# Performance work log

Measured on AMD Instinct MI355X. Metric: run time of the kernel, lower is better.

Reference implementation:

```python
import jax, jax.numpy as jnp
import numpy as np

B, T, M = 4, 1024, 512
H, K, V = 8, 64, 64
EPS = 1e-6


def setup_inputs() -> dict:
    key = jax.random.key(0)
    ks = jax.random.split(key, 8)
    s = 1.0 / np.sqrt(M)
    return {
        "query": jax.random.normal(ks[0], (B, T, M), jnp.float32),
        "key": jax.random.normal(ks[1], (B, T, M), jnp.float32),
        "value": jax.random.normal(ks[2], (B, T, M), jnp.float32),
        "Wq": jax.random.normal(ks[3], (M, H * K), jnp.float32) * s,
        "Wk": jax.random.normal(ks[4], (M, H * K), jnp.float32) * s,
        "Wv": jax.random.normal(ks[5], (M, H * V), jnp.float32) * s,
        # gate linear is zero-initialized in the original (Constant(0.0)); use
        # small random weights so the gate path is exercised numerically.
        "Wg": jax.random.normal(ks[6], (M, H * V), jnp.float32) * (0.02 * s),
        "bg": jnp.zeros((H * V,), jnp.float32),
        "Wo": jax.random.normal(ks[7], (H * V, M), jnp.float32) * (1.0 / np.sqrt(H * V)),
    }


def _phi(x):
    return jax.nn.elu(x) + 1.0


def reference(query, key, value, Wq, Wk, Wv, Wg, bg, Wo):
    # projections -> [B, T, H, d]
    q = (query @ Wq).reshape(B, T, H, K)
    k = (key @ Wk).reshape(B, T, H, K)
    v = (value @ Wv).reshape(B, T, H, V)

    qf = _phi(q)
    kf = _phi(k)

    # multiplicative value gate from the raw value input
    gate = jax.nn.sigmoid((value @ Wg + bg).reshape(B, T, H, V))
    v = v * (2.0 * gate)

    # visualization attention map: qf . kf, causal, row-normalized
    scores = jnp.einsum("bthk,bshk->bhts", qf, kf)  # [B,H,T,T]
    causal = (jnp.arange(T)[None, :] <= jnp.arange(T)[:, None]).astype(scores.dtype)
    scores = scores * causal[None, None]
    att_map = scores / (jnp.sum(scores, axis=-1, keepdims=True) + EPS)

    # causal linear attention via cumulative sums (Tq == Tk so the idx-take
    # in the original is an identity gather)
    kv = jnp.einsum("bthk,bthv->bthkv", kf, v)  # [B,T,H,K,V]
    kv_cum = jnp.cumsum(kv, axis=1)
    k_cum = jnp.cumsum(kf, axis=1)               # [B,T,H,K]

    numer = jnp.einsum("bthk,bthkv->bthv", qf, kv_cum)
    denom = jnp.einsum("bthk,bthk->bth", qf, k_cum) + EPS
    out = (numer / denom[..., None]).reshape(B, T, H * V)
    out = out @ Wo  # [B,T,M]
    return out, att_map
```

## Files before the change

### kernel.cpp

```cpp
#include <hip/hip_runtime.h>
#include <cstdint>

#define TDIM 1024
#define BDIM 4
#define EPSF 1e-6f

#define OFF_INV   0u
#define OFF_KSUM  32768u
#define OFF_KV    65536u
#define FLOAT_BYTES 8650752u
#define UOFF_QP 0u
#define UOFF_KP 2097152u
#define UOFF_VP 4194304u
#define UOFF_NB 6291456u
#define UOFF_WQ 8388608u
#define UOFF_WK 8650752u
#define UOFF_WV 8912896u
#define UOFF_WG 9175040u
#define UOFF_WO 9437184u

typedef short bf16x8 __attribute__((ext_vector_type(8)));
typedef float f32x4  __attribute__((ext_vector_type(4)));
typedef unsigned short ushort_t;

union bfu { int4 i4; unsigned short us[8]; bf16x8 v; };

__device__ __forceinline__ float phi_f(float x)  { return x > 0.f ? x + 1.f : __expf(x); }
__device__ __forceinline__ float sigm_f(float x) { return 1.f / (1.f + __expf(-x)); }
__device__ __forceinline__ unsigned short f2b(float x) {
    union { float f; unsigned u; } v; v.f = x;
    return (unsigned short)((v.u + 0x7FFFu + ((v.u >> 16) & 1u)) >> 16);
}
__device__ __forceinline__ float b2f(unsigned short s) {
    union { unsigned u; float f; } v; v.u = (unsigned)s << 16; return v.f;
}
__device__ __forceinline__ int4 pack8(float4 a, float4 b) {
    bfu u;
    u.us[0] = f2b(a.x); u.us[1] = f2b(a.y); u.us[2] = f2b(a.z); u.us[3] = f2b(a.w);
    u.us[4] = f2b(b.x); u.us[5] = f2b(b.y); u.us[6] = f2b(b.z); u.us[7] = f2b(b.w);
    return u.i4;
}
#define FMA4(ACC, S, V) do { (ACC).x += (S)*(V).x; (ACC).y += (S)*(V).y; \
                             (ACC).z += (S)*(V).z; (ACC).w += (S)*(V).w; } while (0)

__global__ __launch_bounds__(256) void castwt_all(const float* __restrict__ W0,
                                                  const float* __restrict__ W1,
                                                  const float* __restrict__ W2,
                                                  const float* __restrict__ W3,
                                                  const float* __restrict__ W4,
                                                  ushort_t* __restrict__ T0,
                                                  ushort_t* __restrict__ T1,
                                                  ushort_t* __restrict__ T2,
                                                  ushort_t* __restrict__ T3,
                                                  ushort_t* __restrict__ T4) {
    const float* W; ushort_t* Wt;
    switch (blockIdx.z) {
        case 0: W = W0; Wt = T0; break;
        case 1: W = W1; Wt = T1; break;
        case 2: W = W2; Wt = T2; break;
        case 3: W = W3; Wt = T3; break;
        default: W = W4; Wt = T4; break;
    }
    __shared__ unsigned short tile[32][36];
    const int t = threadIdx.x;
    const int r0 = blockIdx.y * 32, c0 = blockIdx.x * 32;
    {
        const int r = t >> 3, c4 = (t & 7) * 4;
        float4 x = *(const float4*)(W + (size_t)(r0 + r) * 512 + c0 + c4);
        tile[c4 + 0][r] = f2b(x.x); tile[c4 + 1][r] = f2b(x.y);
        tile[c4 + 2][r] = f2b(x.z); tile[c4 + 3][r] = f2b(x.w);
    }
    __syncthreads();
    const int c = t >> 3, r4 = (t & 7) * 4;
    ushort4 o;
    o.x = tile[c][r4 + 0]; o.y = tile[c][r4 + 1];
    o.z = tile[c][r4 + 2]; o.w = tile[c][r4 + 3];
    *(ushort4*)(Wt + (size_t)(c0 + c) * 512 + r0 + r4) = o;
}

__global__ __launch_bounds__(256) void proj_k(const float* __restrict__ query,
                                              const float* __restrict__ key_,
                                              const float* __restrict__ value,
                                              const ushort_t* __restrict__ wqt,
                                              const ushort_t* __restrict__ wkt,
                                              const ushort_t* __restrict__ wvt,
                                              const ushort_t* __restrict__ wgt,
                                              const float* __restrict__ bg,
                                              ushort_t* __restrict__ qp,
                                              ushort_t* __restrict__ kp,
                                              ushort_t* __restrict__ vp) {
    __shared__ __align__(16) unsigned short As[2][4096];
    __shared__ __align__(16) unsigned short Bs[2][4096];
    __shared__ __align__(16) unsigned short Bs2[2][4096];
    const int z = blockIdx.z;
    const float* A = (z == 0) ? query : (z == 1) ? key_ : value;
    const ushort_t* B0 = (z == 0) ? wqt : (z == 1) ? wkt : wvt;
    ushort_t* outp = (z == 0) ? qp : (z == 1) ? kp : vp;
    const bool dual = (z == 2);

    const int tid = threadIdx.x;
    const int row0 = blockIdx.x * 64, n0 = blockIdx.y * 64;
    const int w = tid >> 6, lane = tid & 63;
    const int cc = tid & 7, rr = tid >> 3;
    const int fm = lane & 15, fq = lane >> 4;
    const int la0 = (cc * 64 + (rr ^ cc)) * 8;
    const int la1 = (cc * 64 + ((rr + 32) ^ cc)) * 8;

    f32x4 acc[4], acc2[4];
#pragma unroll
    for (int i = 0; i < 4; i++) {
        acc[i]  = (f32x4){0.f, 0.f, 0.f, 0.f};
        acc2[i] = (f32x4){0.f, 0.f, 0.f, 0.f};
    }

    const float*   aptr = A  + (size_t)(row0 + rr) * 512 + cc * 8;
    const ushort_t* bptr = B0 + (size_t)(n0 + rr) * 512 + cc * 8;
    const ushort_t* gptr = wgt + (size_t)(n0 + rr) * 512 + cc * 8;

    float4 a0 = *(const float4*)(aptr);
    float4 a1 = *(const float4*)(aptr + 4);
    float4 a2 = *(const float4*)(aptr + 32 * 512);
    float4 a3 = *(const float4*)(aptr + 32 * 512 + 4);
    int4 b0 = *(const int4*)(bptr);
    int4 b1 = *(const int4*)(bptr + 32 * 512);
    int4 g0 = {0, 0, 0, 0}, g1 = {0, 0, 0, 0};
    if (dual) { g0 = *(const int4*)(gptr); g1 = *(const int4*)(gptr + 32 * 512); }
    *(int4*)&As[0][la0] = pack8(a0, a1);
    *(int4*)&As[0][la1] = pack8(a2, a3);
    *(int4*)&Bs[0][la0] = b0; *(int4*)&Bs[0][la1] = b1;
    if (dual) { *(int4*)&Bs2[0][la0] = g0; *(int4*)&Bs2[0][la1] = g1; }
    __syncthreads();

    for (int kti = 0; kti < 8; kti++) {
        const int buf = kti & 1;
        if (kti < 7) {
            const int off = (kti + 1) * 64;
            a0 = *(const float4*)(aptr + off);
            a1 = *(const float4*)(aptr + off + 4);
            a2 = *(const float4*)(aptr + off + 32 * 512);
            a3 = *(const float4*)(aptr + off + 32 * 512 + 4);
            b0 = *(const int4*)(bptr + off);
            b1 = *(const int4*)(bptr + off + 32 * 512);
            if (dual) {
                g0 = *(const int4*)(gptr + off);
                g1 = *(const int4*)(gptr + off + 32 * 512);
            }
        }
        if (dual) {
#pragma unroll
            for (int j = 0; j < 2; j++) {
                const int cu = j * 4 + fq;
                bf16x8 af = *(const bf16x8*)&As[buf][(cu * 64 + ((w * 16 + fm) ^ cu)) * 8];
#pragma unroll
                for (int nb = 0; nb < 4; nb++) {
                    bf16x8 bv = *(const bf16x8*)&Bs[buf][(cu * 64 + ((nb * 16 + fm) ^ cu)) * 8];
                    bf16x8 gv = *(const bf16x8*)&Bs2[buf][(cu * 64 + ((nb * 16 + fm) ^ cu)) * 8];
                    acc[nb]  = __builtin_amdgcn_mfma_f32_16x16x32_bf16(af, bv, acc[nb], 0, 0, 0);
                    acc2[nb] = __builtin_amdgcn_mfma_f32_16x16x32_bf16(af, gv, acc2[nb], 0, 0, 0);
                }
            }
        } else {
#pragma unroll
            for (int j = 0; j < 2; j++) {
                const int cu = j * 4 + fq;
                bf16x8 af = *(const bf16x8*)&As[buf][(cu * 64 + ((w * 16 + fm) ^ cu)) * 8];
#pragma unroll
                for (int nb = 0; nb < 4; nb++) {
                    bf16x8 bv = *(const bf16x8*)&Bs[buf][(cu * 64 + ((nb * 16 + fm) ^ cu)) * 8];
                    acc[nb] = __builtin_amdgcn_mfma_f32_16x16x32_bf16(af, bv, acc[nb], 0, 0, 0);
                }
            }
        }
        if (kti < 7) {
            const int nb_ = buf ^ 1;
            *(int4*)&As[nb_][la0] = pack8(a0, a1);
            *(int4*)&As[nb_][la1] = pack8(a2, a3);
            *(int4*)&Bs[nb_][la0] = b0; *(int4*)&Bs[nb_][la1] = b1;
            if (dual) { *(int4*)&Bs2[nb_][la0] = g0; *(int4*)&Bs2[nb_][la1] = g1; }
            __syncthreads();
        }
    }

#pragma unroll
    for (int nb = 0; nb < 4; nb++) {
        const int col = n0 + nb * 16 + fm;
        const float bb = dual ? bg[col] : 0.f;
#pragma unroll
        for (int r = 0; r < 4; r++) {
            const int row = row0 + w * 16 + fq * 4 + r;
            const float v = acc[nb][r];
            const ushort_t o = dual ? f2b(v * 2.f * sigm_f(acc2[nb][r] + bb))
                                    : f2b(phi_f(v));
            outp[(size_t)row * 512 + col] = o;
        }
    }
}

__global__ __launch_bounds__(256) void outproj_k(const ushort_t* __restrict__ A,
                                                 const ushort_t* __restrict__ Bt,
                                                 float* __restrict__ out) {
    __shared__ __align__(16) unsigned short As[2][4096];
    __shared__ __align__(16) unsigned short Bs[2][4096];
    const int tid = threadIdx.x;
    const int row0 = blockIdx.x * 64, n0 = blockIdx.y * 64;
    const int w = tid >> 6, lane = tid & 63;
    const int cc = tid & 7, rr = tid >> 3;
    const int fm = lane & 15, fq = lane >> 4;
    const int la0 = (cc * 64 + (rr ^ cc)) * 8;
    const int la1 = (cc * 64 + ((rr + 32) ^ cc)) * 8;

    f32x4 acc[4];
#pragma unroll
    for (int i = 0; i < 4; i++) acc[i] = (f32x4){0.f, 0.f, 0.f, 0.f};

    const ushort_t* aptr = A  + (size_t)(row0 + rr) * 512 + cc * 8;
    const ushort_t* bptr = Bt + (size_t)(n0 + rr) * 512 + cc * 8;
    int4 ra0 = *(const int4*)(aptr);
    int4 ra1 = *(const int4*)(aptr + 32 * 512);
    int4 rb0 = *(const int4*)(bptr);
    int4 rb1 = *(const int4*)(bptr + 32 * 512);
    *(int4*)&As[0][la0] = ra0; *(int4*)&As[0][la1] = ra1;
    *(int4*)&Bs[0][la0] = rb0; *(int4*)&Bs[0][la1] = rb1;
    __syncthreads();

    for (int kti = 0; kti < 8; kti++) {
        const int buf = kti & 1;
        if (kti < 7) {
            const int off = (kti + 1) * 64;
            ra0 = *(const int4*)(aptr + off);
            ra1 = *(const int4*)(aptr + off + 32 * 512);
            rb0 = *(const int4*)(bptr + off);
            rb1 = *(const int4*)(bptr + off + 32 * 512);
        }
#pragma unroll
        for (int j = 0; j < 2; j++) {
            const int cu = j * 4 + fq;
            bf16x8 af = *(const bf16x8*)&As[buf][(cu * 64 + ((w * 16 + fm) ^ cu)) * 8];
#pragma unroll
            for (int nb = 0; nb < 4; nb++) {
                bf16x8 bv = *(const bf16x8*)&Bs[buf][(cu * 64 + ((nb * 16 + fm) ^ cu)) * 8];
                acc[nb] = __builtin_amdgcn_mfma_f32_16x16x32_bf16(af, bv, acc[nb], 0, 0, 0);
            }
        }
        if (kti < 7) {
            const int nb_ = buf ^ 1;
            *(int4*)&As[nb_][la0] = ra0; *(int4*)&As[nb_][la1] = ra1;
            *(int4*)&Bs[nb_][la0] = rb0; *(int4*)&Bs[nb_][la1] = rb1;
            __syncthreads();
        }
    }
#pragma unroll
    for (int nb = 0; nb < 4; nb++) {
        const int col = n0 + nb * 16 + fm;
#pragma unroll
        for (int r = 0; r < 4; r++) {
            const int row = row0 + w * 16 + fq * 4 + r;
            __builtin_nontemporal_store(acc[nb][r], &out[(size_t)row * 512 + col]);
        }
    }
}

__global__ __launch_bounds__(256) void chunksum_k(const ushort_t* __restrict__ kb,
                                                  const ushort_t* __restrict__ vb,
                                                  float* __restrict__ kv,
                                                  float* __restrict__ ksum) {
    __shared__ __align__(16) float kf_c[64][68];
    __shared__ __align__(16) float vg_c[64][68];
    const int tid = threadIdx.x;
    const int bh = blockIdx.x, c = blockIdx.y;
    const int b = bh >> 3, h = bh & 7;
    const int r = tid >> 2, qq = tid & 3;
    {
        const size_t rowbase = ((size_t)(b * TDIM + c * 64 + r)) * 512 + h * 64 + qq * 16;
        bfu k0, k1, v0, v1;
        k0.i4 = *(const int4*)(kb + rowbase);
        k1.i4 = *(const int4*)(kb + rowbase + 8);
        v0.i4 = *(const int4*)(vb + rowbase);
        v1.i4 = *(const int4*)(vb + rowbase + 8);
#pragma unroll
        for (int j = 0; j < 8; j++) {
            kf_c[r][qq * 16 + j]     = b2f(k0.us[j]);
            kf_c[r][qq * 16 + 8 + j] = b2f(k1.us[j]);
            vg_c[r][qq * 16 + j]     = b2f(v0.us[j]);
            vg_c[r][qq * 16 + 8 + j] = b2f(v1.us[j]);
        }
    }
    __syncthreads();
    const int k0i = (tid >> 4) * 4;
    const int v0i = (tid & 15) * 4;
    float4 a4[4];
#pragma unroll
    for (int i = 0; i < 4; i++) a4[i] = make_float4(0.f, 0.f, 0.f, 0.f);
    for (int t = 0; t < 64; t++) {
        float4 kk4 = *(const float4*)&kf_c[t][k0i];
        float4 vv  = *(const float4*)&vg_c[t][v0i];
        FMA4(a4[0], kk4.x, vv); FMA4(a4[1], kk4.y, vv);
        FMA4(a4[2], kk4.z, vv); FMA4(a4[3], kk4.w, vv);
    }
    const size_t base = (size_t)(bh * 16 + c) * 64;
#pragma unroll
    for (int i = 0; i < 4; i++)
        *(float4*)(kv + (base + k0i + i) * 64 + v0i) = a4[i];
    if (tid < 64) {
        float s = 0.f;
        for (int t = 0; t < 64; t++) s += kf_c[t][tid];
        ksum[base + tid] = s;
    }
}

__global__ __launch_bounds__(256) void fused_k(const ushort_t* __restrict__ qb,
                                               const ushort_t* __restrict__ kb,
                                               const ushort_t* __restrict__ vb,
                                               const float* __restrict__ kvc,
                                               const float* __restrict__ ksum,
                                               ushort_t* __restrict__ nbo,
                                               float* __restrict__ invw) {
    __shared__ __align__(16) unsigned short qs[4096];
    __shared__ __align__(16) unsigned short ksb[4096];
    __shared__ __align__(16) unsigned short vrow[64 * 72];
    __shared__ __align__(16) float kvf[64 * 68];
    __shared__ __align__(16) float sc[64 * 68];
    __shared__ float kpre[64];
    __shared__ float ps[256];
    __shared__ float inv_s[64];

    const int tid = threadIdx.x;
    const int bh = blockIdx.x, diag = 15 - (int)blockIdx.y;
    const int tt0 = diag * 64;
    const int b = bh >> 3, h = bh & 7;
    const int w = tid >> 6, lane = tid & 63;
    const int fm = lane & 15, fq = lane >> 4;
    const int rr = tid >> 3, cc = tid & 7;
    const int la0 = (cc * 64 + (rr ^ cc)) * 8;
    const int la1 = (cc * 64 + ((rr + 32) ^ cc)) * 8;

    {
        const ushort_t* qptr = qb + ((size_t)(b * TDIM + tt0 + rr)) * 512 + h * 64 + cc * 8;
        *(int4*)&qs[la0] = *(const int4*)qptr;
        *(int4*)&qs[la1] = *(const int4*)(qptr + 32 * 512);
        const ushort_t* kptr = kb + ((size_t)(b * TDIM + tt0 + rr)) * 512 + h * 64 + cc * 8;
        *(int4*)&ksb[la0] = *(const int4*)kptr;
        *(int4*)&ksb[la1] = *(const int4*)(kptr + 32 * 512);
        const int r = tid >> 2, qq = tid & 3;
        const ushort_t* vptr = vb + ((size_t)(b * TDIM + tt0 + r)) * 512 + h * 64 + qq * 16;
        *(int4*)&vrow[r * 72 + qq * 16]     = *(const int4*)vptr;
        *(int4*)&vrow[r * 72 + qq * 16 + 8] = *(const int4*)(vptr + 8);
        float4 a4[4];
#pragma unroll
        for (int u = 0; u < 4; u++) a4[u] = make_float4(0.f, 0.f, 0.f, 0.f);
        for (int c2 = 0; c2 < diag; c2++) {
            const float* p = kvc + (size_t)(bh * 16 + c2) * 4096 + r * 64 + qq * 16;
#pragma unroll
            for (int u = 0; u < 4; u++) {
                float4 x = *(const float4*)(p + 4 * u);
                a4[u].x += x.x; a4[u].y += x.y; a4[u].z += x.z; a4[u].w += x.w;
            }
        }
#pragma unroll
        for (int u = 0; u < 4; u++) *(float4*)&kvf[r * 68 + qq * 16 + 4 * u] = a4[u];
        if (tid < 64) {
            float s = 0.f;
            for (int c2 = 0; c2 < diag; c2++)
                s += ksum[(size_t)(bh * 16 + c2) * 64 + tid];
            kpre[tid] = s;
        }
    }
    __syncthreads();

    {
        f32x4 sa[4];
#pragma unroll
        for (int i = 0; i < 4; i++) sa[i] = (f32x4){0.f, 0.f, 0.f, 0.f};
#pragma unroll
        for (int j = 0; j < 2; j++) {
            const int cu = j * 4 + fq;
            bf16x8 aqf = *(const bf16x8*)&qs[(cu * 64 + ((w * 16 + fm) ^ cu)) * 8];
#pragma unroll
            for (int nb = 0; nb < 4; nb++) {
                bf16x8 bk = *(const bf16x8*)&ksb[(cu * 64 + ((nb * 16 + fm) ^ cu)) * 8];
                sa[nb] = __builtin_amdgcn_mfma_f32_16x16x32_bf16(aqf, bk, sa[nb], 0, 0, 0);
            }
        }
#pragma unroll
        for (int nb = 0; nb < 4; nb++) {
            const int s_l = nb * 16 + fm;
#pragma unroll
            for (int r = 0; r < 4; r++) {
                const int t_l = w * 16 + fq * 4 + r;
                sc[t_l * 68 + s_l] = (s_l <= t_l) ? sa[nb][r] : 0.f;
            }
        }
    }
    __syncthreads();

    {
        const int rw = tid >> 2, sq = tid & 3;
        float p = 0.f;
#pragma unroll
        for (int s = sq * 16; s < sq * 16 + 16; s++) p += sc[rw * 68 + s];
#pragma unroll
        for (int kd = sq * 16; kd < sq * 16 + 16; kd++) {
            const int cu = kd >> 3;
            p += b2f(qs[(cu * 64 + (rw ^ cu)) * 8 + (kd & 7)]) * kpre[kd];
        }
        ps[rw * 4 + sq] = p;
    }
    __syncthreads();
    {
        const int rw = tid >> 2, sq = tid & 3;
        if (sq == 0) {
            float den = ps[rw * 4] + ps[rw * 4 + 1] + ps[rw * 4 + 2] + ps[rw * 4 + 3];
            const float iv = 1.f / (den + EPSF);
            inv_s[rw] = iv;
            invw[(size_t)(bh * 16 + diag) * 64 + rw] = iv;
        }
    }
    __syncthreads();

    {
        f32x4 oa[4];
#pragma unroll
        for (int i = 0; i < 4; i++) oa[i] = (f32x4){0.f, 0.f, 0.f, 0.f};
        bf16x8 aqv[2], apv[2];
#pragma unroll
        for (int j = 0; j < 2; j++) {
            const int cu = j * 4 + fq;
            aqv[j] = *(const bf16x8*)&qs[(cu * 64 + ((w * 16 + fm) ^ cu)) * 8];
            bfu t;
#pragma unroll
            for (int e2 = 0; e2 < 8; e2++) t.us[e2] = f2b(sc[(w * 16 + fm) * 68 + cu * 8 + e2]);
            apv[j] = t.v;
        }
#pragma unroll
        for (int nb = 0; nb < 4; nb++) {
            const int v = nb * 16 + fm;
#pragma unroll
            for (int j = 0; j < 2; j++) {
                const int cu = j * 4 + fq;
                bfu tkv, tv;
#pragma unroll
                for (int e = 0; e < 8; e++) {
                    tkv.us[e] = f2b(kvf[(cu * 8 + e) * 68 + v]);
                    tv.us[e]  = vrow[(cu * 8 + e) * 72 + v];
                }
                oa[nb] = __builtin_amdgcn_mfma_f32_16x16x32_bf16(aqv[j], tkv.v, oa[nb], 0, 0, 0);
                oa[nb] = __builtin_amdgcn_mfma_f32_16x16x32_bf16(apv[j], tv.v, oa[nb], 0, 0, 0);
            }
        }
#pragma unroll
        for (int nb = 0; nb < 4; nb++) {
            const int vcol = nb * 16 + fm;
#pragma unroll
            for (int r = 0; r < 4; r++) {
                const int t_l = w * 16 + fq * 4 + r;
                const float val = oa[nb][r] * inv_s[t_l];
                nbo[((size_t)(b * TDIM + tt0 + t_l)) * 512 + h * 64 + vcol] = f2b(val);
            }
        }
    }
}

__global__ __launch_bounds__(256) void attmap_k(const ushort_t* __restrict__ qb,
                                                const ushort_t* __restrict__ kb,
                                                const float* __restrict__ invw,
                                                float* __restrict__ att) {
    const int tid = threadIdx.x;
    const int bh = blockIdx.x, tt = blockIdx.y, st = blockIdx.z;
    float* attb = att + ((size_t)bh * TDIM + (size_t)tt * 64) * TDIM + (size_t)st * 64;

    if (st > tt) {
        const int r = tid >> 2, c0 = (tid & 3) * 4;
        const f32x4 z = (f32x4){0.f, 0.f, 0.f, 0.f};
        float* rp = attb + (size_t)r * TDIM + c0;
#pragma unroll
        for (int i = 0; i < 4; i++)
            __builtin_nontemporal_store(z, (f32x4*)(rp + 16 * i));
        return;
    }

    __shared__ __align__(16) unsigned short qs[4096];
    __shared__ __align__(16) unsigned short ks[4096];
    __shared__ float inv_l[64];
    const int b = bh >> 3, h = bh & 7;
    const int rr = tid >> 3, cc = tid & 7;
    const int la0 = (cc * 64 + (rr ^ cc)) * 8;
    const int la1 = (cc * 64 + ((rr + 32) ^ cc)) * 8;

    const ushort_t* qptr = qb + ((size_t)(b * TDIM + tt * 64 + rr)) * 512 + h * 64 + cc * 8;
    *(int4*)&qs[la0] = *(const int4*)qptr;
    *(int4*)&qs[la1] = *(const int4*)(qptr + 32 * 512);
    const ushort_t* kptr = kb + ((size_t)(b * TDIM + st * 64 + rr)) * 512 + h * 64 + cc * 8;
    *(int4*)&ks[la0] = *(const int4*)kptr;
    *(int4*)&ks[la1] = *(const int4*)(kptr + 32 * 512);
    if (tid < 64) inv_l[tid] = invw[(size_t)(bh * 16 + tt) * 64 + tid];
    __syncthreads();

    const int w = tid >> 6, lane = tid & 63;
    const int fm = lane & 15, fq = lane >> 4;
    f32x4 pa[4];
#pragma unroll
    for (int i = 0; i < 4; i++) pa[i] = (f32x4){0.f, 0.f, 0.f, 0.f};
#pragma unroll
    for (int j = 0; j < 2; j++) {
        const int cu = j * 4 + fq;
        bf16x8 aq = *(const bf16x8*)&qs[(cu * 64 + ((w * 16 + fm) ^ cu)) * 8];
#pragma unroll
        for (int nb = 0; nb < 4; nb++) {
            bf16x8 bk = *(const bf16x8*)&ks[(cu * 64 + ((nb * 16 + fm) ^ cu)) * 8];
            pa[nb] = __builtin_amdgcn_mfma_f32_16x16x32_bf16(aq, bk, pa[nb], 0, 0, 0);
        }
    }
    float invr[4];
#pragma unroll
    for (int r = 0; r < 4; r++) invr[r] = inv_l[w * 16 + fq * 4 + r];
    const bool dg = (st == tt);
#pragma unroll
    for (int nb = 0; nb < 4; nb++) {
        const int s_l = nb * 16 + fm;
#pragma unroll
        for (int r = 0; r < 4; r++) {
            const int t_l = w * 16 + fq * 4 + r;
            float val = pa[nb][r] * invr[r];
            if (dg && s_l > t_l) val = 0.f;
            __builtin_nontemporal_store(val, &attb[(size_t)t_l * TDIM + s_l]);
        }
    }
}

extern "C" void kernel_launch(void* const* d_in, const int* in_sizes, int n_in,
                              void* d_out, int out_size, void* d_ws, size_t ws_size,
                              hipStream_t stream) {
    (void)in_sizes; (void)n_in; (void)out_size; (void)ws_size;
    const float* query = (const float*)d_in[0];
    const float* key   = (const float*)d_in[1];
    const float* value = (const float*)d_in[2];
    const float* Wq    = (const float*)d_in[3];
    const float* Wk    = (const float*)d_in[4];
    const float* Wv    = (const float*)d_in[5];
    const float* Wg    = (const float*)d_in[6];
    const float* bg    = (const float*)d_in[7];
    const float* Wo    = (const float*)d_in[8];
    float* out = (float*)d_out;
    float* att = (float*)d_out + 2097152;
    float* ws  = (float*)d_ws;
    float* invw = ws + OFF_INV;
    float* ksum = ws + OFF_KSUM;
    float* kv   = ws + OFF_KV;
    ushort_t* ub  = (ushort_t*)((char*)d_ws + FLOAT_BYTES);
    ushort_t* qp  = ub + UOFF_QP;
    ushort_t* kp  = ub + UOFF_KP;
    ushort_t* vp  = ub + UOFF_VP;
    ushort_t* nbp = ub + UOFF_NB;
    ushort_t* wqt = ub + UOFF_WQ;
    ushort_t* wkt = ub + UOFF_WK;
    ushort_t* wvt = ub + UOFF_WV;
    ushort_t* wgt = ub + UOFF_WG;
    ushort_t* wot = ub + UOFF_WO;

    dim3 blk(256);
    castwt_all<<<dim3(16, 16, 5), blk, 0, stream>>>(Wq, Wk, Wv, Wg, Wo,
                                                    wqt, wkt, wvt, wgt, wot);
    proj_k<<<dim3(64, 8, 3), blk, 0, stream>>>(query, key, value,
                                               wqt, wkt, wvt, wgt, bg, qp, kp, vp);
    chunksum_k<<<dim3(32, 16), blk, 0, stream>>>(kp, vp, kv, ksum);
    fused_k<<<dim3(32, 16), blk, 0, stream>>>(qp, kp, vp, kv, ksum, nbp, invw);
    attmap_k<<<dim3(32, 16, 16), blk, 0, stream>>>(qp, kp, invw, att);
    outproj_k<<<dim3(64, 8), blk, 0, stream>>>(nbp, wot, out);
}
```

Baseline: 259.3 us.

## Process four key tiles per attmap block with double-buffered K loads

Each attention-map block now covers four consecutive 64-wide key tiles instead of one. The Q tile is loaded once and reused, and the next K tile is prefetched into registers and written to a second LDS buffer while the current tile's MFMAs and stores run. Zero-fill of the upper-triangular tiles is handled inside the same block. This cuts the block count by four and amortizes Q loads, but it reduces parallelism and makes work per block uneven along the causal diagonal.

```diff
diff --git a/kernel.cpp b/kernel.cpp
--- a/kernel.cpp
+++ b/kernel.cpp
@@ -465,21 +465,26 @@
                                                 const float* __restrict__ invw,
                                                 float* __restrict__ att) {
     const int tid = threadIdx.x;
-    const int bh = blockIdx.x, tt = blockIdx.y, st = blockIdx.z;
-    float* attb = att + ((size_t)bh * TDIM + (size_t)tt * 64) * TDIM + (size_t)st * 64;
-
-    if (st > tt) {
-        const int r = tid >> 2, c0 = (tid & 3) * 4;
+    const int bh = blockIdx.x, tt = blockIdx.y, chk = blockIdx.z;
+    const int st0 = chk * 4;
+    float* attrow = att + ((size_t)bh * TDIM + (size_t)tt * 64) * TDIM;
+
+    {
+        const int zbeg = (st0 > tt + 1) ? st0 : (tt + 1);
+        const int r = tid >> 2, q4 = (tid & 3) * 4;
         const f32x4 z = (f32x4){0.f, 0.f, 0.f, 0.f};
-        float* rp = attb + (size_t)r * TDIM + c0;
-#pragma unroll
-        for (int i = 0; i < 4; i++)
-            __builtin_nontemporal_store(z, (f32x4*)(rp + 16 * i));
-        return;
-    }
+        for (int st = zbeg; st < st0 + 4; ++st) {
+            float* rp = attrow + (size_t)r * TDIM + st * 64 + q4;
+#pragma unroll
+            for (int i = 0; i < 4; i++)
+                __builtin_nontemporal_store(z, (f32x4*)(rp + 16 * i));
+        }
+    }
+    if (st0 > tt) return;
+    const int lastC = (st0 + 3 < tt) ? (st0 + 3) : tt;
 
     __shared__ __align__(16) unsigned short qs[4096];
-    __shared__ __align__(16) unsigned short ks[4096];
+    __shared__ __align__(16) unsigned short ks[2][4096];
     __shared__ float inv_l[64];
     const int b = bh >> 3, h = bh & 7;
     const int rr = tid >> 3, cc = tid & 7;
@@ -489,40 +494,64 @@
     const ushort_t* qptr = qb + ((size_t)(b * TDIM + tt * 64 + rr)) * 512 + h * 64 + cc * 8;
     *(int4*)&qs[la0] = *(const int4*)qptr;
     *(int4*)&qs[la1] = *(const int4*)(qptr + 32 * 512);
-    const ushort_t* kptr = kb + ((size_t)(b * TDIM + st * 64 + rr)) * 512 + h * 64 + cc * 8;
-    *(int4*)&ks[la0] = *(const int4*)kptr;
-    *(int4*)&ks[la1] = *(const int4*)(kptr + 32 * 512);
+    const ushort_t* kbase = kb + ((size_t)(b * TDIM + rr)) * 512 + h * 64 + cc * 8;
+    {
+        const size_t off = (size_t)st0 * 64 * 512;
+        *(int4*)&ks[0][la0] = *(const int4*)(kbase + off);
+        *(int4*)&ks[0][la1] = *(const int4*)(kbase + off + 32 * 512);
+    }
     if (tid < 64) inv_l[tid] = invw[(size_t)(bh * 16 + tt) * 64 + tid];
     __syncthreads();
 
     const int w = tid >> 6, lane = tid & 63;
     const int fm = lane & 15, fq = lane >> 4;
-    f32x4 pa[4];
-#pragma unroll
-    for (int i = 0; i < 4; i++) pa[i] = (f32x4){0.f, 0.f, 0.f, 0.f};
+    bf16x8 aq[2];
 #pragma unroll
     for (int j = 0; j < 2; j++) {
         const int cu = j * 4 + fq;
-        bf16x8 aq = *(const bf16x8*)&qs[(cu * 64 + ((w * 16 + fm) ^ cu)) * 8];
+        aq[j] = *(const bf16x8*)&qs[(cu * 64 + ((w * 16 + fm) ^ cu)) * 8];
+    }
+    float invr[4];
+#pragma unroll
+    for (int r = 0; r < 4; r++) invr[r] = inv_l[w * 16 + fq * 4 + r];
+
+    int4 rk0, rk1;
+    int bufsel = 0;
+    for (int st = st0; st <= lastC; ++st, bufsel ^= 1) {
+        if (st < lastC) {
+            const size_t off = (size_t)(st + 1) * 64 * 512;
+            rk0 = *(const int4*)(kbase + off);
+            rk1 = *(const int4*)(kbase + off + 32 * 512);
+        }
+        f32x4 pa[4];
+#pragma unroll
+        for (int i = 0; i < 4; i++) pa[i] = (f32x4){0.f, 0.f, 0.f, 0.f};
+#pragma unroll
+        for (int j = 0; j < 2; j++) {
+            const int cu = j * 4 + fq;
+#pragma unroll
+            for (int nb = 0; nb < 4; nb++) {
+                bf16x8 bk = *(const bf16x8*)&ks[bufsel][(cu * 64 + ((nb * 16 + fm) ^ cu)) * 8];
+                pa[nb] = __builtin_amdgcn_mfma_f32_16x16x32_bf16(aq[j], bk, pa[nb], 0, 0, 0);
+            }
+        }
+        const bool dg = (st == tt);
 #pragma unroll
         for (int nb = 0; nb < 4; nb++) {
-            bf16x8 bk = *(const bf16x8*)&ks[(cu * 64 + ((nb * 16 + fm) ^ cu)) * 8];
-            pa[nb] = __builtin_amdgcn_mfma_f32_16x16x32_bf16(aq, bk, pa[nb], 0, 0, 0);
-        }
-    }
-    float invr[4];
-#pragma unroll
-    for (int r = 0; r < 4; r++) invr[r] = inv_l[w * 16 + fq * 4 + r];
-    const bool dg = (st == tt);
-#pragma unroll
-    for (int nb = 0; nb < 4; nb++) {
-        const int s_l = nb * 16 + fm;
-#pragma unroll
-        for (int r = 0; r < 4; r++) {
-            const int t_l = w * 16 + fq * 4 + r;
-            float val = pa[nb][r] * invr[r];
-            if (dg && s_l > t_l) val = 0.f;
-            __builtin_nontemporal_store(val, &attb[(size_t)t_l * TDIM + s_l]);
+            const int s_l = nb * 16 + fm;
+#pragma unroll
+            for (int r = 0; r < 4; r++) {
+                const int t_l = w * 16 + fq * 4 + r;
+                float val = pa[nb][r] * invr[r];
+                if (dg && s_l > t_l) val = 0.f;
+                __builtin_nontemporal_store(val,
+                    &attrow[(size_t)t_l * TDIM + st * 64 + s_l]);
+            }
+        }
+        if (st < lastC) {
+            *(int4*)&ks[bufsel ^ 1][la0] = rk0;
+            *(int4*)&ks[bufsel ^ 1][la1] = rk1;
+            __syncthreads();
         }
     }
 }
@@ -564,6 +593,6 @@
                                                wqt, wkt, wvt, wgt, bg, qp, kp, vp);
     chunksum_k<<<dim3(32, 16), blk, 0, stream>>>(kp, vp, kv, ksum);
     fused_k<<<dim3(32, 16), blk, 0, stream>>>(qp, kp, vp, kv, ksum, nbp, invw);
-    attmap_k<<<dim3(32, 16, 16), blk, 0, stream>>>(qp, kp, invw, att);
+    attmap_k<<<dim3(32, 16, 4), blk, 0, stream>>>(qp, kp, invw, att);
     outproj_k<<<dim3(64, 8), blk, 0, stream>>>(nbp, wot, out);
 }
```

New measurement: 257.3 us. About the same (-0.8%).
